# Kernel tuning notes

Measured on AMD Instinct MI355X. Metric: run time of the kernel, lower is better.

Reference implementation:

```python
import jax, jax.numpy as jnp
import numpy as np

EPS = 1e-5

def _neighbor_idx(H, W):
    # flat index of the 3x3 clamped neighborhood for each pixel, [H*W, 9]
    r = np.arange(H)[:, None, None]  # [H,1,1]
    c = np.arange(W)[None, :, None]  # [1,W,1]
    dr = np.repeat(np.array([-1, 0, 1]), 3)[None, None, :]  # [1,1,9]
    dc = np.tile(np.array([-1, 0, 1]), 3)[None, None, :]
    ri = np.clip(r + dr, 0, H - 1)
    ci = np.clip(c + dc, 0, W - 1)
    return jnp.asarray((ri * W + ci).reshape(H * W, 9))

def setup_inputs() -> dict:
    key = jax.random.key(0)
    ks = jax.random.split(key, 7)
    B, C, H, W = 16, 256, 80, 80
    s = 1.0 / np.sqrt(C)
    return {
        "x": jax.random.normal(ks[0], (B, C, H, W), jnp.float32),
        "Wq": jax.random.normal(ks[1], (C, C), jnp.float32) * s,
        "bq": jax.random.normal(ks[2], (C,), jnp.float32) * s,
        "Wk": jax.random.normal(ks[3], (C, C), jnp.float32) * s,
        "bk": jax.random.normal(ks[4], (C,), jnp.float32) * s,
        "Wv": jax.random.normal(ks[5], (C, C), jnp.float32) * s,
        "bv": jax.random.normal(ks[6], (C,), jnp.float32) * s,
    }

def reference(x, Wq, bq, Wk, bk, Wv, bv):
    B, C, H, W = x.shape
    N = H * W
    xf = x.reshape(B, C, N)
    # 1x1 convs as channel GEMMs
    q = jnp.einsum('oc,bcn->bno', Wq, xf) + bq          # [B,N,C]
    k = jnp.einsum('oc,bcn->bon', Wk, xf) + bk[:, None]  # [B,C,N]
    v = jnp.einsum('oc,bcn->bon', Wv, xf) + bv[:, None]  # [B,C,N]
    idx = _neighbor_idx(H, W)                            # [N,9]
    k_n = k[:, :, idx]                                   # [B,C,N,9]
    v_n = v[:, :, idx]                                   # [B,C,N,9]
    # raw attention scores (NOT softmaxed before AV, matching the source)
    scores = jnp.einsum('bnc,bcnq->bnq', q, k_n)         # [B,N,9]
    new_v = jnp.einsum('bnq,bcnq->bcn', scores, v_n).reshape(B, C, H, W)
    out9 = scores.reshape(B, H, W, 9)
    center = out9[..., 4]
    others_mean = (out9.sum(-1) - center) / 8.0
    output = jnp.stack([center, others_mean], axis=-1)   # [B,H,W,2]
    # residual + layer_norm over [H,W] (no affine), per (B,C)
    xr = x + new_v
    mu = xr.mean(axis=(-2, -1), keepdims=True)
    var = ((xr - mu) ** 2).mean(axis=(-2, -1), keepdims=True)
    x_out = (xr - mu) * jax.lax.rsqrt(var + EPS)
    return (output, x_out)
```

## Files before the change

### kernel.cpp

```cpp
#include <hip/hip_runtime.h>
#include <hip/hip_bf16.h>

using f32x4  = __attribute__((ext_vector_type(4))) float;
using short8 = __attribute__((ext_vector_type(8))) short;
using bf16   = __hip_bfloat16;

constexpr int BATCH = 16;
constexpr int CH    = 256;
constexpr int HH    = 80;
constexpr int WW    = 80;
constexpr int NPIX  = HH * WW;

__device__ __forceinline__ float b2f(unsigned short u) {
    union { unsigned int i; float f; } x;
    x.i = ((unsigned int)u) << 16;
    return x.f;
}

typedef __attribute__((address_space(3))) void  lds_void;
typedef __attribute__((address_space(1))) const void glb_void;
__device__ __forceinline__ void glds16(const void* g, void* l) {
    __builtin_amdgcn_global_load_lds((glb_void*)(unsigned long long)g,
                                     (lds_void*)(unsigned int)(unsigned long long)l,
                                     16, 0, 0);
}

__global__ __launch_bounds__(256) void convert_w(
    const float* __restrict__ Wq, const float* __restrict__ Wk,
    const float* __restrict__ Wv, bf16* __restrict__ Wb)
{
    const int elem = blockIdx.x * 256 + threadIdx.x;
    const int mat  = blockIdx.y;
    const float* src = (mat == 0) ? Wq : (mat == 1) ? Wk : Wv;
    Wb[(size_t)mat * CH * CH + elem] = __float2bfloat16(src[elem]);
}

__global__ __launch_bounds__(256) void transpose_cast(
    const float* __restrict__ x, bf16* __restrict__ xt, int b0)
{
    __shared__ float t[64][65];
    const int b  = b0 + blockIdx.z;
    const int n0 = blockIdx.x * 64;
    const int c0 = blockIdx.y * 64;
    const float* xb = x + (size_t)b * CH * NPIX;
    const int tid = threadIdx.x;

    {
        const int nl  = tid & 63;
        const int cl0 = tid >> 6;
        #pragma unroll
        for (int i = 0; i < 16; ++i) {
            const int cl = cl0 + i * 4;
            t[cl][nl] = xb[(size_t)(c0 + cl) * NPIX + n0 + nl];
        }
    }
    __syncthreads();
    {
        bf16* xtb = xt + (size_t)blockIdx.z * NPIX * CH;
        const int cp  = (tid & 15) * 4;
        const int nl0 = tid >> 4;
        #pragma unroll
        for (int i = 0; i < 4; ++i) {
            const int nl = nl0 + i * 16;
            ushort4 pk;
            #pragma unroll
            for (int j = 0; j < 4; ++j) {
                const bf16 h = __float2bfloat16(t[cp + j][nl]);
                ((unsigned short*)&pk)[j] = *(const unsigned short*)&h;
            }
            *(ushort4*)(xtb + (size_t)(n0 + nl) * CH + c0 + cp) = pk;
        }
    }
}

__global__ __launch_bounds__(256, 2) void qkv_mfma(
    const bf16* __restrict__ xt, const bf16* __restrict__ Wb,
    const float* __restrict__ bq, const float* __restrict__ bk,
    const float* __restrict__ bv,
    bf16* __restrict__ qt, bf16* __restrict__ kt, bf16* __restrict__ vt)
{
    const int bl = blockIdx.z;
    const int n0 = blockIdx.x * 128;
    const int o0 = blockIdx.y * 128;
    const bf16* A = xt + (size_t)bl * NPIX * CH;

    __shared__ char As[128 * 512];
    __shared__ char Bs[2][128 * 64];

    const int tid = threadIdx.x;
    const int wv  = tid >> 6, ln = tid & 63;
    const int wr  = wv >> 1,  wc = wv & 1;
    const int lm  = ln & 15,  lk = ln >> 4;

    #pragma unroll
    for (int t = 0; t < 16; ++t) {
        const int idx = t * 256 + tid;
        const int row = idx >> 5, pos = idx & 31;
        const int chk = pos ^ (row & 7);
        glds16(A + (size_t)(n0 + row) * CH + chk * 8, &As[idx * 16]);
    }

    auto stageB = [&](int buf, const bf16* Wm, int k0) {
        #pragma unroll
        for (int it = 0; it < 2; ++it) {
            const int idx = it * 256 + tid;
            const int row = idx >> 2, pos = idx & 3;
            const int chk = pos ^ ((row >> 1) & 3);
            glds16(Wm + (size_t)(o0 + row) * CH + k0 + chk * 8, &Bs[buf][idx * 16]);
        }
    };

    stageB(0, Wb, 0);
    int buf = 0;

    bf16* const outs[3] = { qt + (size_t)bl * CH * NPIX,
                            kt + (size_t)bl * CH * NPIX,
                            vt + (size_t)bl * CH * NPIX };
    const float* const biases[3] = { bq, bk, bv };

    #pragma unroll
    for (int m = 0; m < 3; ++m) {
        f32x4 acc[4][4];
        #pragma unroll
        for (int i = 0; i < 4; ++i)
            #pragma unroll
            for (int j = 0; j < 4; ++j)
                #pragma unroll
                for (int r = 0; r < 4; ++r) acc[i][j][r] = 0.f;

        #pragma unroll
        for (int t = 0; t < 8; ++t) {
            __syncthreads();
            const int s = m * 8 + t;
            if (s < 23) {
                const int ns = s + 1;
                stageB(buf ^ 1, Wb + (size_t)(ns >> 3) * CH * CH, (ns & 7) * 32);
            }

            short8 afr[4], bfr[4];
            #pragma unroll
            for (int i = 0; i < 4; ++i) {
                const int row = wr * 64 + i * 16 + lm;
                const int chunk = (t * 4 + lk) ^ (row & 7);
                afr[i] = *(const short8*)&As[row * 512 + chunk * 16];
            }
            #pragma unroll
            for (int j = 0; j < 4; ++j) {
                const int row = wc * 64 + j * 16 + lm;
                const int chk = lk ^ ((row >> 1) & 3);
                bfr[j] = *(const short8*)&Bs[buf][row * 64 + chk * 16];
            }
            #pragma unroll
            for (int i = 0; i < 4; ++i)
                #pragma unroll
                for (int j = 0; j < 4; ++j)
                    acc[i][j] = __builtin_amdgcn_mfma_f32_16x16x32_bf16(
                        afr[i], bfr[j], acc[i][j], 0, 0, 0);
            buf ^= 1;
        }

        bf16* out = outs[m];
        const float* bias = biases[m];
        #pragma unroll
        for (int j = 0; j < 4; ++j) {
            const int o = o0 + wc * 64 + j * 16 + lm;
            const float bs = bias[o];
            #pragma unroll
            for (int i = 0; i < 4; ++i) {
                const int nb = n0 + wr * 64 + i * 16 + lk * 4;
                ushort4 pk;
                #pragma unroll
                for (int r = 0; r < 4; ++r) {
                    const bf16 h = __float2bfloat16(acc[i][j][r] + bs);
                    ((unsigned short*)&pk)[r] = *(const unsigned short*)&h;
                }
                *(ushort4*)(out + (size_t)o * NPIX + nb) = pk;
            }
        }
    }
}

__global__ __launch_bounds__(256) void scores_kernel(
    const bf16* __restrict__ qt, const bf16* __restrict__ kt,
    float* __restrict__ scores, float* __restrict__ out0, int b0)
{
    const int tid   = threadIdx.x;
    const int wave  = tid >> 6;
    const int lane  = tid & 63;
    const int ql    = lane & 15;
    const int chunk = lane >> 4;

    const int qi = blockIdx.x * 64 + wave * 16 + ql;
    const int bl = blockIdx.y;
    const int b  = b0 + bl;
    const int n0 = qi * 4;
    const int r  = qi / 20;
    const int p0 = n0 - r * WW;

    const unsigned short* qp = (const unsigned short*)(qt + (size_t)bl * NPIX * CH)
                               + (size_t)chunk * 64 * NPIX;
    const unsigned short* kp = (const unsigned short*)(kt + (size_t)bl * NPIX * CH)
                               + (size_t)chunk * 64 * NPIX;

    const int rbm = max(r - 1, 0) * WW;
    const int rb0 = r * WW;
    const int rbp = min(r + 1, HH - 1) * WW;
    const bool eL = (p0 == 0), eR = (p0 == 76);

    float acc[4][9];
    #pragma unroll
    for (int px = 0; px < 4; ++px)
        #pragma unroll
        for (int j = 0; j < 9; ++j) acc[px][j] = 0.f;

    for (int c = 0; c < 64; ++c) {
        const size_t cb = (size_t)c * NPIX;
        const ushort4 qv = *(const ushort4*)(qp + cb + n0);
        const float qf0 = b2f(qv.x), qf1 = b2f(qv.y), qf2 = b2f(qv.z), qf3 = b2f(qv.w);

        #pragma unroll
        for (int dr = 0; dr < 3; ++dr) {
            const int rb = (dr == 0) ? rbm : (dr == 1) ? rb0 : rbp;
            const unsigned short* kr = kp + cb + rb + p0;
            const ushort2 wl  = *(const ushort2*)(kr - 2);
            const ushort4 wm  = *(const ushort4*)(kr);
            const ushort2 wr2 = *(const ushort2*)(kr + 4);
            const float w3 = b2f(wl.y);
            const float w4 = b2f(wm.x), w5 = b2f(wm.y), w6 = b2f(wm.z), w7 = b2f(wm.w);
            const float w8 = b2f(wr2.x);

            acc[0][dr*3+0] += qf0 * w3;
            acc[0][dr*3+1] += qf0 * w4;
            acc[0][dr*3+2] += qf0 * w5;
            acc[1][dr*3+0] += qf1 * w4;
            acc[1][dr*3+1] += qf1 * w5;
            acc[1][dr*3+2] += qf1 * w6;
            acc[2][dr*3+0] += qf2 * w5;
            acc[2][dr*3+1] += qf2 * w6;
            acc[2][dr*3+2] += qf2 * w7;
            acc[3][dr*3+0] += qf3 * w6;
            acc[3][dr*3+1] += qf3 * w7;
            acc[3][dr*3+2] += qf3 * w8;
            if (eL) acc[0][dr*3+0] += qf0 * (w4 - w3);
            if (eR) acc[3][dr*3+2] += qf3 * (w7 - w8);
        }
    }

    #pragma unroll
    for (int px = 0; px < 4; ++px)
        #pragma unroll
        for (int j = 0; j < 9; ++j) {
            float v = acc[px][j];
            v += __shfl_xor(v, 16, 64);
            v += __shfl_xor(v, 32, 64);
            acc[px][j] = v;
        }

    float* sp = scores + (size_t)bl * 9 * NPIX;
    if (chunk < 3) {
        #pragma unroll
        for (int jj = 0; jj < 3; ++jj) {
            const int j = chunk * 3 + jj;
            float4 v = { acc[0][j], acc[1][j], acc[2][j], acc[3][j] };
            *(float4*)(sp + (size_t)j * NPIX + n0) = v;
        }
    } else {
        float ssum[4];
        #pragma unroll
        for (int px = 0; px < 4; ++px) {
            float s = 0.f;
            #pragma unroll
            for (int j = 0; j < 9; ++j) s += acc[px][j];
            ssum[px] = s;
        }
        float* op = out0 + ((size_t)b * NPIX + n0) * 2;
        float4 o0v = { acc[0][4], (ssum[0] - acc[0][4]) * 0.125f,
                       acc[1][4], (ssum[1] - acc[1][4]) * 0.125f };
        float4 o1v = { acc[2][4], (ssum[2] - acc[2][4]) * 0.125f,
                       acc[3][4], (ssum[3] - acc[3][4]) * 0.125f };
        *(float4*)(op)     = o0v;
        *(float4*)(op + 4) = o1v;
    }
}

__global__ __launch_bounds__(320) void newv_ln(
    const float* __restrict__ x, const bf16* __restrict__ vt,
    const float* __restrict__ scores, float* __restrict__ xout, int b0)
{
    __shared__ __align__(16) unsigned short lds_v[NPIX];
    __shared__ float rsum[5], rsq[5];

    const int c  = blockIdx.x;
    const int bl = blockIdx.y;
    const int b  = b0 + bl;
    const int tid = threadIdx.x;

    const unsigned short* vrow = (const unsigned short*)(vt + ((size_t)bl * CH + c) * NPIX);
    const float* xrow = x + ((size_t)b * CH + c) * NPIX;
    const float* sb   = scores + (size_t)bl * 9 * NPIX;

    #pragma unroll
    for (int i = 0; i < 3; ++i) {
        const int t = tid + i * 320;
        if (t < NPIX / 8) ((int4*)lds_v)[t] = ((const int4*)vrow)[t];
    }
    __syncthreads();

    float val[20];
    float sum = 0.f, sq = 0.f;
    #pragma unroll
    for (int it = 0; it < 5; ++it) {
        const int p   = tid + it * 320;
        const int n0  = p * 4;
        const int r   = p / 20;
        const int c0  = (p % 20) * 4;

        const int rm = max(r - 1, 0) * WW;
        const int r0 = r * WW;
        const int rp = min(r + 1, HH - 1) * WW;

        float4 s[9];
        #pragma unroll
        for (int j = 0; j < 9; ++j)
            s[j] = *(const float4*)(sb + (size_t)j * NPIX + n0);

        const float4 xin = *(const float4*)(xrow + n0);

        const int cA = max(c0 - 1, 0);
        const int cF = min(c0 + 4, WW - 1);
        float vm[6], v0[6], vp[6];
        vm[0] = b2f(lds_v[rm + cA]); v0[0] = b2f(lds_v[r0 + cA]); vp[0] = b2f(lds_v[rp + cA]);
        #pragma unroll
        for (int t = 1; t < 5; ++t) {
            vm[t] = b2f(lds_v[rm + c0 + t - 1]);
            v0[t] = b2f(lds_v[r0 + c0 + t - 1]);
            vp[t] = b2f(lds_v[rp + c0 + t - 1]);
        }
        vm[5] = b2f(lds_v[rm + cF]); v0[5] = b2f(lds_v[r0 + cF]); vp[5] = b2f(lds_v[rp + cF]);

        #pragma unroll
        for (int px = 0; px < 4; ++px) {
            const float sc0 = ((const float*)&s[0])[px];
            const float sc1 = ((const float*)&s[1])[px];
            const float sc2 = ((const float*)&s[2])[px];
            const float sc3 = ((const float*)&s[3])[px];
            const float sc4 = ((const float*)&s[4])[px];
            const float sc5 = ((const float*)&s[5])[px];
            const float sc6 = ((const float*)&s[6])[px];
            const float sc7 = ((const float*)&s[7])[px];
            const float sc8 = ((const float*)&s[8])[px];
            float a;
            a  = sc0 * vm[px] + sc1 * vm[px + 1] + sc2 * vm[px + 2];
            a += sc3 * v0[px] + sc4 * v0[px + 1] + sc5 * v0[px + 2];
            a += sc6 * vp[px] + sc7 * vp[px + 1] + sc8 * vp[px + 2];
            const float vv = ((const float*)&xin)[px] + a;
            val[it * 4 + px] = vv;
            sum += vv;
            sq  += vv * vv;
        }
    }

    #pragma unroll
    for (int off = 32; off >= 1; off >>= 1) {
        sum += __shfl_xor(sum, off, 64);
        sq  += __shfl_xor(sq,  off, 64);
    }
    const int wave = tid >> 6, lane = tid & 63;
    if (lane == 0) { rsum[wave] = sum; rsq[wave] = sq; }
    __syncthreads();
    sum = rsum[0] + rsum[1] + rsum[2] + rsum[3] + rsum[4];
    sq  = rsq[0]  + rsq[1]  + rsq[2]  + rsq[3]  + rsq[4];

    const float mu   = sum * (1.f / NPIX);
    const float var  = sq * (1.f / NPIX) - mu * mu;
    const float rstd = rsqrtf(var + 1e-5f);

    float* orow = xout + ((size_t)b * CH + c) * NPIX;
    #pragma unroll
    for (int it = 0; it < 5; ++it) {
        const int n0 = (tid + it * 320) * 4;
        float4 o;
        o.x = (val[it * 4 + 0] - mu) * rstd;
        o.y = (val[it * 4 + 1] - mu) * rstd;
        o.z = (val[it * 4 + 2] - mu) * rstd;
        o.w = (val[it * 4 + 3] - mu) * rstd;
        *(float4*)(orow + n0) = o;
    }
}

extern "C" void kernel_launch(void* const* d_in, const int* in_sizes, int n_in,
                              void* d_out, int out_size, void* d_ws, size_t ws_size,
                              hipStream_t stream)
{
    const float* x  = (const float*)d_in[0];
    const float* Wq = (const float*)d_in[1];
    const float* bq = (const float*)d_in[2];
    const float* Wk = (const float*)d_in[3];
    const float* bk = (const float*)d_in[4];
    const float* Wv = (const float*)d_in[5];
    const float* bv = (const float*)d_in[6];

    float* out0 = (float*)d_out;
    float* xout = out0 + (size_t)BATCH * NPIX * 2;

    char* ws = (char*)d_ws;
    bf16* Wb = (bf16*)ws;
    ws += (size_t)3 * CH * CH * sizeof(bf16);

    const size_t fBF = (size_t)NPIX * CH * sizeof(bf16);
    const size_t fSC = (size_t)NPIX * 9 * sizeof(float);
    const size_t perBatch = 4 * fBF + fSC;

    size_t avail = ws_size - ((size_t)3 * CH * CH * sizeof(bf16));
    int NB = (int)(avail / perBatch);
    if (NB < 1)  NB = 1;
    if (NB > BATCH) NB = BATCH;

    bf16*  xt  = (bf16*)ws;
    bf16*  qtb = (bf16*)(ws + (size_t)NB * fBF);
    bf16*  ktb = (bf16*)(ws + (size_t)NB * fBF * 2);
    bf16*  vtb = (bf16*)(ws + (size_t)NB * fBF * 3);
    float* sc  = (float*)(ws + (size_t)NB * fBF * 4);

    convert_w<<<dim3(CH * CH / 256, 3), 256, 0, stream>>>(Wq, Wk, Wv, Wb);

    for (int b0 = 0; b0 < BATCH; b0 += NB) {
        const int cnb = (BATCH - b0 < NB) ? (BATCH - b0) : NB;

        transpose_cast<<<dim3(NPIX / 64, CH / 64, cnb), 256, 0, stream>>>(x, xt, b0);

        qkv_mfma<<<dim3(NPIX / 128, CH / 128, cnb), 256, 0, stream>>>(
            xt, Wb, bq, bk, bv, qtb, ktb, vtb);

        scores_kernel<<<dim3(NPIX / 256, cnb), 256, 0, stream>>>(qtb, ktb, sc, out0, b0);

        newv_ln<<<dim3(CH, cnb), 320, 0, stream>>>(x, vtb, sc, xout, b0);
    }
}
```

Measured before the change: 309.3 us.

## Split scores channel reduction 8-way and process two channels per newv_ln block

The scores kernel now splits the 256-channel dot product across 8 lane groups of 32 channels instead of 4 of 64. Each block covers 32 pixel quads, and a single 16-byte load replaces three smaller loads per neighbor row, giving more blocks and shorter serial loops at the cost of an extra shuffle stage. The newv_ln kernel now handles two channels per block, so each score tile load is reused for two channels and the number of blocks is halved. In exchange, per-thread register use grows.

```diff
diff --git a/kernel.cpp b/kernel.cpp
--- a/kernel.cpp
+++ b/kernel.cpp
@@ -187,10 +187,10 @@
     const int tid   = threadIdx.x;
     const int wave  = tid >> 6;
     const int lane  = tid & 63;
-    const int ql    = lane & 15;
-    const int chunk = lane >> 4;
-
-    const int qi = blockIdx.x * 64 + wave * 16 + ql;
+    const int ql    = lane & 7;
+    const int chunk = lane >> 3;
+
+    const int qi = blockIdx.x * 32 + wave * 8 + ql;
     const int bl = blockIdx.y;
     const int b  = b0 + bl;
     const int n0 = qi * 4;
@@ -198,9 +198,9 @@
     const int p0 = n0 - r * WW;
 
     const unsigned short* qp = (const unsigned short*)(qt + (size_t)bl * NPIX * CH)
-                               + (size_t)chunk * 64 * NPIX;
+                               + (size_t)chunk * 32 * NPIX;
     const unsigned short* kp = (const unsigned short*)(kt + (size_t)bl * NPIX * CH)
-                               + (size_t)chunk * 64 * NPIX;
+                               + (size_t)chunk * 32 * NPIX;
 
     const int rbm = max(r - 1, 0) * WW;
     const int rb0 = r * WW;
@@ -213,7 +213,8 @@
         #pragma unroll
         for (int j = 0; j < 9; ++j) acc[px][j] = 0.f;
 
-    for (int c = 0; c < 64; ++c) {
+    #pragma unroll 4
+    for (int c = 0; c < 32; ++c) {
         const size_t cb = (size_t)c * NPIX;
         const ushort4 qv = *(const ushort4*)(qp + cb + n0);
         const float qf0 = b2f(qv.x), qf1 = b2f(qv.y), qf2 = b2f(qv.z), qf3 = b2f(qv.w);
@@ -221,13 +222,13 @@
         #pragma unroll
         for (int dr = 0; dr < 3; ++dr) {
             const int rb = (dr == 0) ? rbm : (dr == 1) ? rb0 : rbp;
-            const unsigned short* kr = kp + cb + rb + p0;
-            const ushort2 wl  = *(const ushort2*)(kr - 2);
-            const ushort4 wm  = *(const ushort4*)(kr);
-            const ushort2 wr2 = *(const ushort2*)(kr + 4);
-            const float w3 = b2f(wl.y);
-            const float w4 = b2f(wm.x), w5 = b2f(wm.y), w6 = b2f(wm.z), w7 = b2f(wm.w);
-            const float w8 = b2f(wr2.x);
+            const short8 kw = *(const short8*)(kp + cb + rb + p0 - 2);
+            const float w3 = b2f((unsigned short)kw[1]);
+            const float w4 = b2f((unsigned short)kw[2]);
+            const float w5 = b2f((unsigned short)kw[3]);
+            const float w6 = b2f((unsigned short)kw[4]);
+            const float w7 = b2f((unsigned short)kw[5]);
+            const float w8 = b2f((unsigned short)kw[6]);
 
             acc[0][dr*3+0] += qf0 * w3;
             acc[0][dr*3+1] += qf0 * w4;
@@ -251,20 +252,23 @@
         #pragma unroll
         for (int j = 0; j < 9; ++j) {
             float v = acc[px][j];
+            v += __shfl_xor(v, 8,  64);
             v += __shfl_xor(v, 16, 64);
             v += __shfl_xor(v, 32, 64);
             acc[px][j] = v;
         }
 
     float* sp = scores + (size_t)bl * 9 * NPIX;
-    if (chunk < 3) {
-        #pragma unroll
-        for (int jj = 0; jj < 3; ++jj) {
-            const int j = chunk * 3 + jj;
-            float4 v = { acc[0][j], acc[1][j], acc[2][j], acc[3][j] };
-            *(float4*)(sp + (size_t)j * NPIX + n0) = v;
-        }
+    if (chunk < 7) {
+        float4 v = { acc[0][chunk], acc[1][chunk], acc[2][chunk], acc[3][chunk] };
+        *(float4*)(sp + (size_t)chunk * NPIX + n0) = v;
     } else {
+        float4 v7 = { acc[0][7], acc[1][7], acc[2][7], acc[3][7] };
+        float4 v8 = { acc[0][8], acc[1][8], acc[2][8], acc[3][8] };
+        *(float4*)(sp + (size_t)7 * NPIX + n0) = v7;
+        *(float4*)(sp + (size_t)8 * NPIX + n0) = v8;
+    }
+    if (chunk == 0) {
         float ssum[4];
         #pragma unroll
         for (int px = 0; px < 4; ++px) {
@@ -287,27 +291,26 @@
     const float* __restrict__ x, const bf16* __restrict__ vt,
     const float* __restrict__ scores, float* __restrict__ xout, int b0)
 {
-    __shared__ __align__(16) unsigned short lds_v[NPIX];
-    __shared__ float rsum[5], rsq[5];
-
-    const int c  = blockIdx.x;
-    const int bl = blockIdx.y;
-    const int b  = b0 + bl;
+    __shared__ __align__(16) unsigned short lds_v[2][NPIX];
+    __shared__ float rsum[5][2], rsq[5][2];
+
+    const int cp2 = blockIdx.x;
+    const int bl  = blockIdx.y;
+    const int b   = b0 + bl;
     const int tid = threadIdx.x;
 
-    const unsigned short* vrow = (const unsigned short*)(vt + ((size_t)bl * CH + c) * NPIX);
-    const float* xrow = x + ((size_t)b * CH + c) * NPIX;
-    const float* sb   = scores + (size_t)bl * 9 * NPIX;
-
-    #pragma unroll
-    for (int i = 0; i < 3; ++i) {
-        const int t = tid + i * 320;
-        if (t < NPIX / 8) ((int4*)lds_v)[t] = ((const int4*)vrow)[t];
-    }
+    const int4* vsrc = (const int4*)(vt + ((size_t)bl * CH + cp2 * 2) * NPIX);
+    const float* xrow0 = x + ((size_t)b * CH + cp2 * 2) * NPIX;
+    const float* xrow1 = xrow0 + NPIX;
+    const float* sb    = scores + (size_t)bl * 9 * NPIX;
+
+    #pragma unroll
+    for (int i = 0; i < 5; ++i)
+        ((int4*)lds_v)[tid + i * 320] = vsrc[tid + i * 320];
     __syncthreads();
 
-    float val[20];
-    float sum = 0.f, sq = 0.f;
+    float val0[20], val1[20];
+    float sum0 = 0.f, sq0 = 0.f, sum1 = 0.f, sq1 = 0.f;
     #pragma unroll
     for (int it = 0; it < 5; ++it) {
         const int p   = tid + it * 320;
@@ -324,67 +327,83 @@
         for (int j = 0; j < 9; ++j)
             s[j] = *(const float4*)(sb + (size_t)j * NPIX + n0);
 
-        const float4 xin = *(const float4*)(xrow + n0);
+        const float4 xin0 = *(const float4*)(xrow0 + n0);
+        const float4 xin1 = *(const float4*)(xrow1 + n0);
 
         const int cA = max(c0 - 1, 0);
         const int cF = min(c0 + 4, WW - 1);
-        float vm[6], v0[6], vp[6];
-        vm[0] = b2f(lds_v[rm + cA]); v0[0] = b2f(lds_v[r0 + cA]); vp[0] = b2f(lds_v[rp + cA]);
-        #pragma unroll
-        for (int t = 1; t < 5; ++t) {
-            vm[t] = b2f(lds_v[rm + c0 + t - 1]);
-            v0[t] = b2f(lds_v[r0 + c0 + t - 1]);
-            vp[t] = b2f(lds_v[rp + c0 + t - 1]);
-        }
-        vm[5] = b2f(lds_v[rm + cF]); v0[5] = b2f(lds_v[r0 + cF]); vp[5] = b2f(lds_v[rp + cF]);
-
-        #pragma unroll
-        for (int px = 0; px < 4; ++px) {
-            const float sc0 = ((const float*)&s[0])[px];
-            const float sc1 = ((const float*)&s[1])[px];
-            const float sc2 = ((const float*)&s[2])[px];
-            const float sc3 = ((const float*)&s[3])[px];
-            const float sc4 = ((const float*)&s[4])[px];
-            const float sc5 = ((const float*)&s[5])[px];
-            const float sc6 = ((const float*)&s[6])[px];
-            const float sc7 = ((const float*)&s[7])[px];
-            const float sc8 = ((const float*)&s[8])[px];
-            float a;
-            a  = sc0 * vm[px] + sc1 * vm[px + 1] + sc2 * vm[px + 2];
-            a += sc3 * v0[px] + sc4 * v0[px + 1] + sc5 * v0[px + 2];
-            a += sc6 * vp[px] + sc7 * vp[px + 1] + sc8 * vp[px + 2];
-            const float vv = ((const float*)&xin)[px] + a;
-            val[it * 4 + px] = vv;
-            sum += vv;
-            sq  += vv * vv;
+
+        #pragma unroll
+        for (int pl = 0; pl < 2; ++pl) {
+            const unsigned short* lv = lds_v[pl];
+            float vm[6], v0[6], vp[6];
+            vm[0] = b2f(lv[rm + cA]); v0[0] = b2f(lv[r0 + cA]); vp[0] = b2f(lv[rp + cA]);
+            #pragma unroll
+            for (int t = 1; t < 5; ++t) {
+                vm[t] = b2f(lv[rm + c0 + t - 1]);
+                v0[t] = b2f(lv[r0 + c0 + t - 1]);
+                vp[t] = b2f(lv[rp + c0 + t - 1]);
+            }
+            vm[5] = b2f(lv[rm + cF]); v0[5] = b2f(lv[r0 + cF]); vp[5] = b2f(lv[rp + cF]);
+
+            const float4 xin = pl ? xin1 : xin0;
+            #pragma unroll
+            for (int px = 0; px < 4; ++px) {
+                float a;
+                a  = ((const float*)&s[0])[px] * vm[px]
+                   + ((const float*)&s[1])[px] * vm[px + 1]
+                   + ((const float*)&s[2])[px] * vm[px + 2];
+                a += ((const float*)&s[3])[px] * v0[px]
+                   + ((const float*)&s[4])[px] * v0[px + 1]
+                   + ((const float*)&s[5])[px] * v0[px + 2];
+                a += ((const float*)&s[6])[px] * vp[px]
+                   + ((const float*)&s[7])[px] * vp[px + 1]
+                   + ((const float*)&s[8])[px] * vp[px + 2];
+                const float vv = ((const float*)&xin)[px] + a;
+                if (pl == 0) { val0[it * 4 + px] = vv; sum0 += vv; sq0 += vv * vv; }
+                else         { val1[it * 4 + px] = vv; sum1 += vv; sq1 += vv * vv; }
+            }
         }
     }
 
     #pragma unroll
     for (int off = 32; off >= 1; off >>= 1) {
-        sum += __shfl_xor(sum, off, 64);
-        sq  += __shfl_xor(sq,  off, 64);
+        sum0 += __shfl_xor(sum0, off, 64);
+        sq0  += __shfl_xor(sq0,  off, 64);
+        sum1 += __shfl_xor(sum1, off, 64);
+        sq1  += __shfl_xor(sq1,  off, 64);
     }
     const int wave = tid >> 6, lane = tid & 63;
-    if (lane == 0) { rsum[wave] = sum; rsq[wave] = sq; }
+    if (lane == 0) {
+        rsum[wave][0] = sum0; rsq[wave][0] = sq0;
+        rsum[wave][1] = sum1; rsq[wave][1] = sq1;
+    }
     __syncthreads();
-    sum = rsum[0] + rsum[1] + rsum[2] + rsum[3] + rsum[4];
-    sq  = rsq[0]  + rsq[1]  + rsq[2]  + rsq[3]  + rsq[4];
-
-    const float mu   = sum * (1.f / NPIX);
-    const float var  = sq * (1.f / NPIX) - mu * mu;
-    const float rstd = rsqrtf(var + 1e-5f);
-
-    float* orow = xout + ((size_t)b * CH + c) * NPIX;
+    sum0 = rsum[0][0] + rsum[1][0] + rsum[2][0] + rsum[3][0] + rsum[4][0];
+    sq0  = rsq[0][0]  + rsq[1][0]  + rsq[2][0]  + rsq[3][0]  + rsq[4][0];
+    sum1 = rsum[0][1] + rsum[1][1] + rsum[2][1] + rsum[3][1] + rsum[4][1];
+    sq1  = rsq[0][1]  + rsq[1][1]  + rsq[2][1]  + rsq[3][1]  + rsq[4][1];
+
+    const float mu0   = sum0 * (1.f / NPIX);
+    const float var0  = sq0 * (1.f / NPIX) - mu0 * mu0;
+    const float rstd0 = rsqrtf(var0 + 1e-5f);
+    const float mu1   = sum1 * (1.f / NPIX);
+    const float var1  = sq1 * (1.f / NPIX) - mu1 * mu1;
+    const float rstd1 = rsqrtf(var1 + 1e-5f);
+
+    float* orow0 = xout + ((size_t)b * CH + cp2 * 2) * NPIX;
+    float* orow1 = orow0 + NPIX;
     #pragma unroll
     for (int it = 0; it < 5; ++it) {
         const int n0 = (tid + it * 320) * 4;
-        float4 o;
-        o.x = (val[it * 4 + 0] - mu) * rstd;
-        o.y = (val[it * 4 + 1] - mu) * rstd;
-        o.z = (val[it * 4 + 2] - mu) * rstd;
-        o.w = (val[it * 4 + 3] - mu) * rstd;
-        *(float4*)(orow + n0) = o;
+        float4 o0, o1;
+        #pragma unroll
+        for (int px = 0; px < 4; ++px) {
+            ((float*)&o0)[px] = (val0[it * 4 + px] - mu0) * rstd0;
+            ((float*)&o1)[px] = (val1[it * 4 + px] - mu1) * rstd1;
+        }
+        *(float4*)(orow0 + n0) = o0;
+        *(float4*)(orow1 + n0) = o1;
     }
 }
 
@@ -432,8 +451,8 @@
         qkv_mfma<<<dim3(NPIX / 128, CH / 128, cnb), 256, 0, stream>>>(
             xt, Wb, bq, bk, bv, qtb, ktb, vtb);
 
-        scores_kernel<<<dim3(NPIX / 256, cnb), 256, 0, stream>>>(qtb, ktb, sc, out0, b0);
-
-        newv_ln<<<dim3(CH, cnb), 320, 0, stream>>>(x, vtb, sc, xout, b0);
-    }
-}
+        scores_kernel<<<dim3(50, cnb), 256, 0, stream>>>(qtb, ktb, sc, out0, b0);
+
+        newv_ln<<<dim3(CH / 2, cnb), 320, 0, stream>>>(x, vtb, sc, xout, b0);
+    }
+}
```

Result: faster. 272.8 us (-11.8%).
